# Kernel optimization log

Measured on AMD Instinct MI355X. Metric: run time of the kernel, lower is better.

## Reference

```python
import jax, jax.numpy as jnp
import numpy as np

E = 768      # embed_dim
H = 12       # num_heads
D = E // H   # head_dim = 64
G = 8        # num_groups (grouped 1x1 conv)
MAX_S = 197  # max_seq_len
RED = 8      # SE reduction ratio
S, B = 197, 64


def grouped_linear(x, w, b):
    """Grouped 1x1 conv as grouped linear. x: [..., Cin], w: [Cout, Cin//G], b: [Cout]."""
    cout = w.shape[0]
    cin = x.shape[-1]
    xg = x.reshape(x.shape[:-1] + (G, cin // G))
    wg = w.reshape(G, cout // G, cin // G)
    y = jnp.einsum('...gi,goi->...go', xg, wg)
    return y.reshape(x.shape[:-1] + (cout,)) + b


def channel_shuffle(x):
    """Shuffle channels (last dim) across G groups, matching torch channel_shuffle."""
    c = x.shape[-1]
    xg = x.reshape(x.shape[:-1] + (G, c // G))
    return jnp.swapaxes(xg, -1, -2).reshape(x.shape)


def layernorm(x, g, b, eps=1e-5):
    mu = jnp.mean(x, axis=-1, keepdims=True)
    var = jnp.var(x, axis=-1, keepdims=True)
    return (x - mu) * jax.lax.rsqrt(var + eps) * g + b


def setup_inputs() -> dict:
    rng = jax.random.key(0)
    ks = jax.random.split(rng, 16)
    std = 0.02
    return {
        'query': jax.random.normal(ks[0], (S, B, E), jnp.float32),
        'key':   jax.random.normal(ks[1], (S, B, E), jnp.float32),
        'value': jax.random.normal(ks[2], (S, B, E), jnp.float32),
        'qkv_w': jax.random.normal(ks[3], (3 * E, E // G), jnp.float32) * std,
        'qkv_b': jnp.zeros((3 * E,), jnp.float32),
        'out_w': jax.random.normal(ks[4], (E, E // G), jnp.float32) * std,
        'out_b': jnp.zeros((E,), jnp.float32),
        'rel_pos': jax.random.normal(ks[5], (2 * MAX_S - 1, D), jnp.float32) * std,
        'ln_g': jnp.ones((E,), jnp.float32),
        'ln_b': jnp.zeros((E,), jnp.float32),
        'fc1_w': jax.random.normal(ks[6], (E, E // RED), jnp.float32) * std,
        'fc1_b': jnp.zeros((E // RED,), jnp.float32),
        'fc2_w': jax.random.normal(ks[7], (E // RED, E), jnp.float32) * std,
        'fc2_b': jnp.zeros((E,), jnp.float32),
    }


def reference(query, key, value, qkv_w, qkv_b, out_w, out_b, rel_pos,
              ln_g, ln_b, fc1_w, fc1_b, fc2_w, fc2_b):
    seq_len, bsz, embed_dim = query.shape
    scaling = float(D) ** -0.5

    x = jnp.transpose(query, (1, 0, 2))              # [B, S, E]
    qkv = grouped_linear(x, qkv_w, qkv_b)            # [B, S, 3E]
    qkv = channel_shuffle(qkv)                       # [B, S, 3E]
    q, k, v = jnp.split(qkv, 3, axis=-1)             # each [B, S, E]

    def heads(t):                                    # [B, S, E] -> [B, H, S, D]
        return jnp.transpose(t.reshape(bsz, seq_len, H, D), (0, 2, 1, 3))
    q, k, v = heads(q) * scaling, heads(k), heads(v)

    attn_w = jnp.einsum('bhsd,bhtd->bhst', q, k)     # content-content

    # decoupled relative-position attention (note: slice, not skew, per source)
    rel = rel_pos[MAX_S - seq_len: MAX_S + seq_len - 1]           # [2S-1, D]
    content_pos = jnp.einsum('bhsd,rd->bhsr', q, rel)[..., seq_len - 1: 2 * seq_len - 1]
    pos_content = jnp.einsum('rd,bhtd->bhrt', rel, k)[:, :, seq_len - 1: 2 * seq_len - 1, :]
    attn_w = attn_w + content_pos + pos_content

    probs = jax.nn.softmax(attn_w, axis=-1)          # [B, H, S, S]
    attn = jnp.einsum('bhst,bhtd->bhsd', probs, v)   # [B, H, S, D]
    attn = jnp.transpose(attn, (0, 2, 1, 3)).reshape(bsz, seq_len, E)  # [B, S, E]

    # squeeze-excite style feature calibration gating
    scale = jax.nn.sigmoid(
        jnp.dot(jax.nn.gelu(jnp.dot(layernorm(attn, ln_g, ln_b), fc1_w) + fc1_b), fc2_w) + fc2_b)
    attn = attn * scale

    out = grouped_linear(attn, out_w, out_b)         # [B, S, E]
    out = jnp.transpose(out, (1, 0, 2))              # [S, B, E]

    avg_weights = jnp.sum(probs, axis=1) / H         # [B, S, S]
    return out, avg_weights
```

## Files before the change

kernel.cpp:

```cpp
#include <hip/hip_runtime.h>
#include <hip/hip_bf16.h>

constexpr int S = 197;
constexpr int B = 64;
constexpr int E = 768;
constexpr int H = 12;
constexpr int D = 64;
constexpr int M = S * B;
constexpr size_t SBE = (size_t)M * E;
constexpr int PST = 208;

typedef short bf16x8 __attribute__((ext_vector_type(8)));
typedef float f32x4 __attribute__((ext_vector_type(4)));
typedef unsigned int u32x4 __attribute__((ext_vector_type(4)));

__device__ __forceinline__ unsigned short f2b(float x) {
  unsigned int u = __float_as_uint(x);
  return (unsigned short)((u + 0x7FFFu + ((u >> 16) & 1u)) >> 16);
}
__device__ __forceinline__ float b2f(unsigned short u) {
  return __uint_as_float((unsigned int)u << 16);
}

__global__ __launch_bounds__(256) void mha_wprep(const float* __restrict__ w1,
                                                 const float* __restrict__ w2,
                                                 const float* __restrict__ lng,
                                                 const float* __restrict__ lnb,
                                                 const float* __restrict__ b1,
                                                 const float* __restrict__ rel,
                                                 const float* __restrict__ wq,
                                                 unsigned short* __restrict__ w1t,
                                                 unsigned short* __restrict__ w2t,
                                                 float* __restrict__ cgb,
                                                 float* __restrict__ cbb,
                                                 unsigned short* __restrict__ relb,
                                                 unsigned short* __restrict__ wqt) {
  const int bid = blockIdx.x, tid = threadIdx.x;
  if (bid < 288) {
    int idx = bid * 256 + tid;
    int n = idx / 768, k = idx - n * 768;
    w1t[idx] = f2b(lng[k] * w1[(size_t)k * 96 + n]);
  } else if (bid < 576) {
    int idx = (bid - 288) * 256 + tid;
    int n = idx / 96, k = idx - n * 96;
    w2t[idx] = f2b(w2[(size_t)k * 768 + n]);
  } else if (bid == 576) {
    if (tid < 96) {
      float cg = 0.f, cb = 0.f;
      for (int k = 0; k < 768; ++k) {
        float wv = w1[(size_t)k * 96 + tid];
        cg += lng[k] * wv;
        cb += lnb[k] * wv;
      }
      cgb[tid] = cg;
      cbb[tid] = cb + b1[tid];
    }
  } else if (bid < 641) {
    int idx = (bid - 577) * 256 + tid;
    int s2 = idx >> 6, d = idx & 63;
    float v = (s2 < S) ? rel[(size_t)(S - 1 + s2) * D + d] : 0.f;
    relb[idx] = f2b(v);
  } else {
    int idx = (bid - 641) * 256 + tid;
    wqt[idx] = f2b(wq[idx]);
  }
}

__global__ __launch_bounds__(256) void mha_xcvt(const float* __restrict__ x,
                                                unsigned short* __restrict__ xb) {
  size_t i = ((size_t)blockIdx.x * 256 + threadIdx.x) * 8;
  float4 v0 = *reinterpret_cast<const float4*>(x + i);
  float4 v1 = *reinterpret_cast<const float4*>(x + i + 4);
  unsigned short o[8] = {f2b(v0.x), f2b(v0.y), f2b(v0.z), f2b(v0.w),
                         f2b(v1.x), f2b(v1.y), f2b(v1.z), f2b(v1.w)};
  *(u32x4*)(xb + i) = *(const u32x4*)o;
}

__global__ __launch_bounds__(256) void mha_qkv_gemm(const unsigned short* __restrict__ xb,
                                                    const unsigned short* __restrict__ wqt,
                                                    const float* __restrict__ bias,
                                                    unsigned short* __restrict__ y) {
  const int m0 = blockIdx.x * 64;
  const int n0 = blockIdx.y * 96;
  const int g = blockIdx.y / 3;
  const int tid = threadIdx.x;
  const int lane = tid & 63, wv = tid >> 6;
  const int l15 = lane & 15, l4 = lane >> 4;

  const unsigned short* xr = xb + (size_t)(m0 + 16 * wv + l15) * E + g * 96 + l4 * 8;
  bf16x8 a0 = *(const bf16x8*)(xr);
  bf16x8 a1 = *(const bf16x8*)(xr + 32);
  bf16x8 a2 = *(const bf16x8*)(xr + 64);

  const int mloc = m0 + 16 * wv + 4 * l4;
#pragma unroll
  for (int nf = 0; nf < 6; ++nf) {
    const unsigned short* wr = wqt + (size_t)(n0 + nf * 16 + l15) * 96 + l4 * 8;
    f32x4 a = (f32x4){0.f, 0.f, 0.f, 0.f};
    a = __builtin_amdgcn_mfma_f32_16x16x32_bf16(a0, *(const bf16x8*)(wr), a, 0, 0, 0);
    a = __builtin_amdgcn_mfma_f32_16x16x32_bf16(a1, *(const bf16x8*)(wr + 32), a, 0, 0, 0);
    a = __builtin_amdgcn_mfma_f32_16x16x32_bf16(a2, *(const bf16x8*)(wr + 64), a, 0, 0, 0);
    int p = n0 + nf * 16 + l15;
    float bv = bias[p];
#pragma unroll
    for (int r = 0; r < 4; ++r)
      y[(size_t)(mloc + r) * 2304 + p] = f2b(a[r] + bv);
  }
}

__global__ __launch_bounds__(256) void mha_qkv_shuffle(const unsigned short* __restrict__ y,
                                                       const float* __restrict__ rel,
                                                       unsigned short* __restrict__ qb,
                                                       unsigned short* __restrict__ kb,
                                                       unsigned short* __restrict__ vb) {
  const int tid = threadIdx.x;
  const int lane = tid & 63;
  const int g = lane >> 3, j = lane & 7;
  const int d = j * 8 + g;
  const int wrow = tid >> 6;
  const int rbase = blockIdx.x * 16;

  float relv[4];
  int sA[4], bA[4];
#pragma unroll
  for (int r8 = 0; r8 < 4; ++r8) {
    int rowl = rbase + r8 * 4 + wrow;
    sA[r8] = rowl >> 6;
    bA[r8] = rowl & 63;
    relv[r8] = rel[(size_t)(S - 1 + sA[r8]) * D + d];
  }

  for (int h = 0; h < H; ++h) {
#pragma unroll
    for (int r8 = 0; r8 < 4; ++r8) {
      int rowl = rbase + r8 * 4 + wrow;
      const unsigned short* yr = y + (size_t)rowl * 2304 + g * 288 + h * 8 + j;
      size_t o = (((size_t)bA[r8] * H + h) * S + sA[r8]) * D + d;
      float vq = b2f(yr[0]);
      float vk = b2f(yr[96]);
      float vv = b2f(yr[192]);
      qb[o] = f2b(0.125f * vq + relv[r8]);
      kb[o] = f2b(vk + relv[r8]);
      vb[o] = f2b(vv);
    }
  }
}

__global__ __launch_bounds__(256) void mha_fattn(
    const unsigned short* __restrict__ qb, const unsigned short* __restrict__ kb,
    const unsigned short* __restrict__ vb, const unsigned short* __restrict__ relb,
    float* __restrict__ context, unsigned short* __restrict__ probs, int bh0) {
  __shared__ __align__(16) unsigned short KtPt[64 * 136];
  __shared__ __align__(16) unsigned short Vh[64 * 136];
  unsigned short* Kt = KtPt;
  unsigned short* Pt = KtPt;

  const int id = blockIdx.x;
  const int xcd = id & 7;
  const int rr = id >> 3;
  const int stile = rr & 3;
  const int bhl = xcd + 8 * (rr >> 2);
  const int bh = bh0 + bhl;
  const int b_ = bh / H, h_ = bh - b_ * H;
  const int s0 = stile * 64;
  const int tid = threadIdx.x;
  const int lane = tid & 63, w = tid >> 6;
  const int l15 = lane & 15, l4 = lane >> 4;
  const int vt = tid & 63;
  const int vdb = (tid >> 6) * 8;

  const unsigned short* qg = qb + (((size_t)bh * S + (s0 + 16 * w + l15)) << 6) + l4 * 8;
  const unsigned short* rg = relb + (((size_t)(s0 + 16 * w + l15)) << 6) + l4 * 8;
  bf16x8 aq0 = *(const bf16x8*)(qg);
  bf16x8 aq1 = *(const bf16x8*)(qg + 32);
  bf16x8 aq2 = *(const bf16x8*)(rg);
  bf16x8 aq3 = *(const bf16x8*)(rg + 32);

  auto loadK = [&](int tc, u32x4* kv, u32x4* rv) {
#pragma unroll
    for (int ii = 0; ii < 2; ++ii) {
      int idx = tid + ii * 256;
      int r = idx >> 3, c = idx & 7;
      int tg = tc * 64 + r;
      kv[ii] = (u32x4){0, 0, 0, 0};
      rv[ii] = (u32x4){0, 0, 0, 0};
      if (tg < S) {
        kv[ii] = *(const u32x4*)(kb + (((size_t)bh * S + tg) << 6) + c * 8);
        u32x4 rvv = *(const u32x4*)(relb + ((size_t)tg << 6) + c * 8);
        rv[ii] = rvv ^ 0x80008000u;
      }
    }
  };

  f32x4 acc[13];
#pragma unroll
  for (int i = 0; i < 13; ++i) acc[i] = (f32x4){0.f, 0.f, 0.f, 0.f};

  u32x4 kvA[2], rvA[2], kvB[2], rvB[2];
  loadK(0, kvA, rvA);

#pragma unroll
  for (int tc = 0; tc < 4; ++tc) {
    u32x4* kvc = (tc & 1) ? kvB : kvA;
    u32x4* rvc = (tc & 1) ? rvB : rvA;
#pragma unroll
    for (int ii = 0; ii < 2; ++ii) {
      int idx = tid + ii * 256;
      int r = idx >> 3, c = idx & 7;
      *(u32x4*)(Kt + r * 136 + c * 8) = kvc[ii];
      *(u32x4*)(Kt + r * 136 + 64 + c * 8) = rvc[ii];
    }
    if (tc < 3) loadK(tc + 1, (tc & 1) ? kvA : kvB, (tc & 1) ? rvA : rvB);
    __syncthreads();
#pragma unroll
    for (int tf = 0; tf < 4; ++tf) {
      if (tc == 3 && tf > 0) continue;
      const unsigned short* kbse = Kt + (tf * 16 + l15) * 136 + l4 * 8;
      f32x4 a = acc[tc * 4 + tf];
      a = __builtin_amdgcn_mfma_f32_16x16x32_bf16(aq0, *(const bf16x8*)(kbse), a, 0, 0, 0);
      a = __builtin_amdgcn_mfma_f32_16x16x32_bf16(aq1, *(const bf16x8*)(kbse + 32), a, 0, 0, 0);
      a = __builtin_amdgcn_mfma_f32_16x16x32_bf16(aq2, *(const bf16x8*)(kbse + 64), a, 0, 0, 0);
      a = __builtin_amdgcn_mfma_f32_16x16x32_bf16(aq3, *(const bf16x8*)(kbse + 96), a, 0, 0, 0);
      acc[tc * 4 + tf] = a;
    }
    __syncthreads();
  }

  u32x4 v1[4];
#pragma unroll
  for (int ii = 0; ii < 4; ++ii) {
    int t = (ii & 1) * 64 + vt;
    int d0 = vdb + (ii >> 1) * 32;
    v1[ii] = *(const u32x4*)(vb + (((size_t)bh * S + t) << 6) + d0);
  }

  if (l15 >= 5) acc[12] = (f32x4){-3.0e38f, -3.0e38f, -3.0e38f, -3.0e38f};
  float inv[4];
#pragma unroll
  for (int r = 0; r < 4; ++r) {
    float m = acc[0][r];
#pragma unroll
    for (int tf = 1; tf < 13; ++tf) m = fmaxf(m, acc[tf][r]);
#pragma unroll
    for (int off = 1; off < 16; off <<= 1) m = fmaxf(m, __shfl_xor(m, off, 64));
    float s = 0.f;
#pragma unroll
    for (int tf = 0; tf < 13; ++tf) {
      float e = __expf(acc[tf][r] - m);
      acc[tf][r] = e;
      s += e;
    }
#pragma unroll
    for (int off = 1; off < 16; off <<= 1) s += __shfl_xor(s, off, 64);
    inv[r] = 1.f / s;
  }

  f32x4 ov[4];
#pragma unroll
  for (int df = 0; df < 4; ++df) ov[df] = (f32x4){0.f, 0.f, 0.f, 0.f};

#pragma unroll
  for (int tf = 0; tf < 8; ++tf)
#pragma unroll
    for (int r = 0; r < 4; ++r)
      Pt[(16 * w + 4 * l4 + r) * 136 + tf * 16 + l15] = f2b(acc[tf][r] * inv[r]);
#pragma unroll
  for (int ii = 0; ii < 4; ++ii) {
    int t = (ii & 1) * 64 + vt;
    int d0 = vdb + (ii >> 1) * 32;
    const unsigned short* vp = (const unsigned short*)&v1[ii];
#pragma unroll
    for (int j = 0; j < 8; ++j) Vh[(d0 + j) * 136 + t] = vp[j];
  }
  __syncthreads();

  u32x4 v2[4];
#pragma unroll
  for (int ii = 0; ii < 4; ++ii) {
    int t = 128 + (ii & 1) * 64 + vt;
    int d0 = vdb + (ii >> 1) * 32;
    v2[ii] = (u32x4){0, 0, 0, 0};
    if (t < S) v2[ii] = *(const u32x4*)(vb + (((size_t)bh * S + t) << 6) + d0);
  }

  {
    const int r2 = tid >> 2;
    const int sg = s0 + r2;
    if (sg < S) {
#pragma unroll
      for (int j = 0; j < 4; ++j) {
        int c = (tid & 3) + 4 * j;
        u32x4 pv = *(const u32x4*)(Pt + r2 * 136 + c * 8);
        *(u32x4*)(probs + ((size_t)bhl * S + sg) * PST + c * 8) = pv;
      }
    }
  }
  {
    bf16x8 ap[4];
#pragma unroll
    for (int kf = 0; kf < 4; ++kf)
      ap[kf] = *(const bf16x8*)(Pt + (16 * w + l15) * 136 + kf * 32 + l4 * 8);
#pragma unroll
    for (int df = 0; df < 4; ++df) {
      const unsigned short* vbse = Vh + (df * 16 + l15) * 136 + l4 * 8;
      f32x4 o = ov[df];
#pragma unroll
      for (int kf = 0; kf < 4; ++kf)
        o = __builtin_amdgcn_mfma_f32_16x16x32_bf16(ap[kf], *(const bf16x8*)(vbse + kf * 32), o, 0, 0, 0);
      ov[df] = o;
    }
  }
  __syncthreads();

#pragma unroll
  for (int tf = 8; tf < 13; ++tf)
#pragma unroll
    for (int r = 0; r < 4; ++r)
      Pt[(16 * w + 4 * l4 + r) * 136 + (tf - 8) * 16 + l15] = f2b(acc[tf][r] * inv[r]);
#pragma unroll
  for (int r = 0; r < 4; ++r)
    Pt[(16 * w + 4 * l4 + r) * 136 + 80 + l15] = 0;
#pragma unroll
  for (int ii = 0; ii < 4; ++ii) {
    int t0h = (ii & 1) * 64 + vt;
    int d0 = vdb + (ii >> 1) * 32;
    if (t0h < 96) {
      const unsigned short* vp = (const unsigned short*)&v2[ii];
#pragma unroll
      for (int j = 0; j < 8; ++j) Vh[(d0 + j) * 136 + t0h] = vp[j];
    }
  }
  __syncthreads();

  {
    const int r2 = tid >> 2;
    const int sg = s0 + r2;
    if (sg < S) {
#pragma unroll
      for (int j = 0; j < 3; ++j) {
        int c = (tid & 3) + 4 * j;
        if (c < 10) {
          u32x4 pv = *(const u32x4*)(Pt + r2 * 136 + c * 8);
          *(u32x4*)(probs + ((size_t)bhl * S + sg) * PST + 128 + c * 8) = pv;
        }
      }
    }
  }
  {
    bf16x8 ap[3];
#pragma unroll
    for (int kf = 0; kf < 3; ++kf)
      ap[kf] = *(const bf16x8*)(Pt + (16 * w + l15) * 136 + kf * 32 + l4 * 8);
#pragma unroll
    for (int df = 0; df < 4; ++df) {
      const unsigned short* vbse = Vh + (df * 16 + l15) * 136 + l4 * 8;
      f32x4 o = ov[df];
#pragma unroll
      for (int kf = 0; kf < 3; ++kf)
        o = __builtin_amdgcn_mfma_f32_16x16x32_bf16(ap[kf], *(const bf16x8*)(vbse + kf * 32), o, 0, 0, 0);
      ov[df] = o;
    }
  }

#pragma unroll
  for (int df = 0; df < 4; ++df)
#pragma unroll
    for (int r = 0; r < 4; ++r) {
      int sg = s0 + 16 * w + 4 * l4 + r;
      if (sg < S)
        context[((size_t)b_ * S + sg) * E + h_ * 64 + df * 16 + l15] = ov[df][r];
    }
}

__global__ __launch_bounds__(256) void mha_avgred(const unsigned short* __restrict__ probs,
                                                  float* __restrict__ avg, int b0) {
  const int bs = blockIdx.x;
  const int bl = bs / S, s = bs - bl * S;
  const int t = threadIdx.x;
  if (t >= S) return;
  float acc = 0.f;
#pragma unroll
  for (int h = 0; h < H; ++h)
    acc += b2f(probs[(((size_t)bl * H + h) * S + s) * PST + t]);
  avg[(((size_t)(b0 + bl)) * S + s) * S + t] = acc * (1.f / H);
}

__global__ __launch_bounds__(128) void mha_fc1ln(const float* __restrict__ ctx,
                                                 const unsigned short* __restrict__ w1t,
                                                 const float* __restrict__ cgb,
                                                 const float* __restrict__ cbb,
                                                 unsigned short* __restrict__ h1) {
  __shared__ __align__(16) unsigned short As[32 * 104];
  __shared__ __align__(16) unsigned short Wl[48 * 104];
  __shared__ float smu[32], sinv[32];
  const int m0 = blockIdx.x * 32;
  const int n0 = blockIdx.y * 48;
  const int tid = threadIdx.x;
  const int lane = tid & 63, w = tid >> 6;
  const int l15 = lane & 15, l4 = lane >> 4;
  const int r = tid >> 2, q = tid & 3;

  float s1 = 0.f, s2 = 0.f;
  f32x4 acc[3];
#pragma unroll
  for (int nf = 0; nf < 3; ++nf) acc[nf] = (f32x4){0.f, 0.f, 0.f, 0.f};

  for (int c = 0; c < 8; ++c) {
    const int k0 = c * 96;
    {
      const float* xr = ctx + (size_t)(m0 + r) * E + k0 + q * 24;
      unsigned short* ar = As + r * 104 + q * 24;
#pragma unroll
      for (int j = 0; j < 6; ++j) {
        float4 v = *reinterpret_cast<const float4*>(xr + j * 4);
        s1 += v.x + v.y + v.z + v.w;
        s2 += v.x * v.x + v.y * v.y + v.z * v.z + v.w * v.w;
        ar[j * 4 + 0] = f2b(v.x); ar[j * 4 + 1] = f2b(v.y);
        ar[j * 4 + 2] = f2b(v.z); ar[j * 4 + 3] = f2b(v.w);
      }
    }
    for (int i = tid; i < 48 * 12; i += 128) {
      int n = i / 12, c8 = i - n * 12;
      *(u32x4*)(Wl + n * 104 + c8 * 8) =
          *(const u32x4*)(w1t + (size_t)(n0 + n) * E + k0 + c8 * 8);
    }
    __syncthreads();
    const unsigned short* arow = As + (16 * w + l15) * 104 + l4 * 8;
    bf16x8 a0 = *(const bf16x8*)(arow);
    bf16x8 a1 = *(const bf16x8*)(arow + 32);
    bf16x8 a2 = *(const bf16x8*)(arow + 64);
#pragma unroll
    for (int nf = 0; nf < 3; ++nf) {
      const unsigned short* wr = Wl + (nf * 16 + l15) * 104 + l4 * 8;
      f32x4 a = acc[nf];
      a = __builtin_amdgcn_mfma_f32_16x16x32_bf16(a0, *(const bf16x8*)(wr), a, 0, 0, 0);
      a = __builtin_amdgcn_mfma_f32_16x16x32_bf16(a1, *(const bf16x8*)(wr + 32), a, 0, 0, 0);
      a = __builtin_amdgcn_mfma_f32_16x16x32_bf16(a2, *(const bf16x8*)(wr + 64), a, 0, 0, 0);
      acc[nf] = a;
    }
    __syncthreads();
  }

  s1 += __shfl_xor(s1, 1, 64); s1 += __shfl_xor(s1, 2, 64);
  s2 += __shfl_xor(s2, 1, 64); s2 += __shfl_xor(s2, 2, 64);
  if (q == 0) {
    float mu = s1 * (1.f / E);
    float var = s2 * (1.f / E) - mu * mu;
    smu[r] = mu;
    sinv[r] = rsqrtf(var + 1e-5f);
  }
  __syncthreads();

#pragma unroll
  for (int nf = 0; nf < 3; ++nf) {
    int n = n0 + nf * 16 + l15;
    float cg = cgb[n], cb = cbb[n];
#pragma unroll
    for (int rr = 0; rr < 4; ++rr) {
      int ml = 16 * w + 4 * l4 + rr;
      float u = sinv[ml] * (acc[nf][rr] - smu[ml] * cg) + cb;
      float gl = 0.5f * u * (1.f + tanhf(0.7978845608028654f * (u + 0.044715f * u * u * u)));
      h1[(size_t)(m0 + ml) * 96 + n] = f2b(gl);
    }
  }
}

__global__ __launch_bounds__(256) void mha_fc2(const unsigned short* __restrict__ h1,
                                               const unsigned short* __restrict__ w2t,
                                               const float* __restrict__ bias,
                                               const float* __restrict__ ctx,
                                               unsigned short* __restrict__ attn2) {
  __shared__ __align__(16) unsigned short Hs[64 * 104];
  __shared__ __align__(16) unsigned short Wl[192 * 104];
  const int m0 = blockIdx.x * 64;
  const int n0 = blockIdx.y * 192;
  const int tid = threadIdx.x;
  const int lane = tid & 63, w = tid >> 6;
  const int l15 = lane & 15, l4 = lane >> 4;

  for (int i = tid; i < 64 * 12; i += 256) {
    int rr = i / 12, c8 = i - rr * 12;
    *(u32x4*)(Hs + rr * 104 + c8 * 8) =
        *(const u32x4*)(h1 + (size_t)(m0 + rr) * 96 + c8 * 8);
  }
  for (int i = tid; i < 192 * 12; i += 256) {
    int n = i / 12, c8 = i - n * 12;
    *(u32x4*)(Wl + n * 104 + c8 * 8) =
        *(const u32x4*)(w2t + (size_t)(n0 + n) * 96 + c8 * 8);
  }
  __syncthreads();

  const unsigned short* arow = Hs + (16 * w + l15) * 104 + l4 * 8;
  bf16x8 a0 = *(const bf16x8*)(arow);
  bf16x8 a1 = *(const bf16x8*)(arow + 32);
  bf16x8 a2 = *(const bf16x8*)(arow + 64);

#pragma unroll
  for (int nf = 0; nf < 12; ++nf) {
    const unsigned short* wr = Wl + (nf * 16 + l15) * 104 + l4 * 8;
    f32x4 a = (f32x4){0.f, 0.f, 0.f, 0.f};
    a = __builtin_amdgcn_mfma_f32_16x16x32_bf16(a0, *(const bf16x8*)(wr), a, 0, 0, 0);
    a = __builtin_amdgcn_mfma_f32_16x16x32_bf16(a1, *(const bf16x8*)(wr + 32), a, 0, 0, 0);
    a = __builtin_amdgcn_mfma_f32_16x16x32_bf16(a2, *(const bf16x8*)(wr + 64), a, 0, 0, 0);
    int n = n0 + nf * 16 + l15;
    float bv = bias[n];
#pragma unroll
    for (int rr = 0; rr < 4; ++rr) {
      int m = m0 + 16 * w + 4 * l4 + rr;
      float val = a[rr] + bv;
      float sg = 1.f / (1.f + __expf(-val));
      float cv = ctx[(size_t)m * E + n];
      attn2[(size_t)m * E + n] = f2b(cv * sg);
    }
  }
}

__global__ __launch_bounds__(256) void mha_out(const unsigned short* __restrict__ attn2,
                                               const float* __restrict__ w,
                                               const float* __restrict__ bias,
                                               float* __restrict__ outp) {
  __shared__ __align__(16) unsigned short Asl[64 * 104];
  __shared__ __align__(16) unsigned short Wl[96 * 104];
  __shared__ float bias_s[96];
  const int m0 = blockIdx.x * 64;
  const int g = blockIdx.y;
  const int n0 = g * 96;
  const int tid = threadIdx.x;
  const int lane = tid & 63, w_ = tid >> 6;
  const int l15 = lane & 15, l4 = lane >> 4;

  for (int i = tid; i < 64 * 12; i += 256) {
    int rr = i / 12, c8 = i - rr * 12;
    *(u32x4*)(Asl + rr * 104 + c8 * 8) =
        *(const u32x4*)(attn2 + (size_t)(m0 + rr) * E + n0 + c8 * 8);
  }
  for (int i = tid; i < 96 * 24; i += 256) {
    int n = i / 24, c4 = i - n * 24;
    float4 v = *reinterpret_cast<const float4*>(&w[(size_t)(n0 + n) * 96 + c4 * 4]);
    unsigned short* dst = Wl + n * 104 + c4 * 4;
    dst[0] = f2b(v.x); dst[1] = f2b(v.y); dst[2] = f2b(v.z); dst[3] = f2b(v.w);
  }
  if (tid < 96) bias_s[tid] = bias[n0 + tid];
  __syncthreads();

  const unsigned short* arow = Asl + (16 * w_ + l15) * 104 + l4 * 8;
  bf16x8 a0 = *(const bf16x8*)(arow);
  bf16x8 a1 = *(const bf16x8*)(arow + 32);
  bf16x8 a2 = *(const bf16x8*)(arow + 64);

  int bb4[4], ss4[4];
#pragma unroll
  for (int rr = 0; rr < 4; ++rr) {
    int m = m0 + 16 * w_ + 4 * l4 + rr;
    bb4[rr] = m / S;
    ss4[rr] = m - bb4[rr] * S;
  }

#pragma unroll
  for (int nf = 0; nf < 6; ++nf) {
    const unsigned short* wr = Wl + (nf * 16 + l15) * 104 + l4 * 8;
    f32x4 a = (f32x4){0.f, 0.f, 0.f, 0.f};
    a = __builtin_amdgcn_mfma_f32_16x16x32_bf16(a0, *(const bf16x8*)(wr), a, 0, 0, 0);
    a = __builtin_amdgcn_mfma_f32_16x16x32_bf16(a1, *(const bf16x8*)(wr + 32), a, 0, 0, 0);
    a = __builtin_amdgcn_mfma_f32_16x16x32_bf16(a2, *(const bf16x8*)(wr + 64), a, 0, 0, 0);
    int p = n0 + nf * 16 + l15;
    float bv = bias_s[p - n0];
#pragma unroll
    for (int rr = 0; rr < 4; ++rr)
      outp[((size_t)ss4[rr] * B + bb4[rr]) * E + p] = a[rr] + bv;
  }
}

extern "C" void kernel_launch(void* const* d_in, const int* in_sizes, int n_in,
                              void* d_out, int out_size, void* d_ws, size_t ws_size,
                              hipStream_t stream) {
  const float* query = (const float*)d_in[0];
  const float* qkv_w = (const float*)d_in[3];
  const float* qkv_b = (const float*)d_in[4];
  const float* out_w = (const float*)d_in[5];
  const float* out_b = (const float*)d_in[6];
  const float* rel   = (const float*)d_in[7];
  const float* ln_g  = (const float*)d_in[8];
  const float* ln_b  = (const float*)d_in[9];
  const float* fc1_w = (const float*)d_in[10];
  const float* fc1_b = (const float*)d_in[11];
  const float* fc2_w = (const float*)d_in[12];
  const float* fc2_b = (const float*)d_in[13];

  float* ws = (float*)d_ws;
  unsigned short* qb   = (unsigned short*)ws;
  unsigned short* xbuf = qb;
  unsigned short* kbuf = qb + SBE;
  unsigned short* vbb  = kbuf + SBE;
  unsigned short* relb = vbb + SBE;
  size_t off = 3 * SBE / 2 + 8192;
  float* context = ws + off;
  unsigned short* attn2b = (unsigned short*)(ws + off + SBE);
  unsigned short* ybuf = (unsigned short*)context;
  unsigned short* h1b = attn2b + SBE;
  unsigned short* w1t = h1b + (size_t)M * 96;
  unsigned short* w2t = w1t + 73728;
  unsigned short* wqt = w2t + 73728;
  float* cgb = (float*)(wqt + 221184);
  float* cbb = cgb + 96;
  unsigned short* probsb = (unsigned short*)(cbb + 96);
  float* outp = (float*)d_out;
  float* avgp = outp + SBE;

  size_t used_f = off + SBE + (SBE + (size_t)M * 96 + 368640) / 2 + 192;
  size_t avail_f = (ws_size / 4 > used_f) ? ws_size / 4 - used_f : 0;
  int Bc = 2;
  const int cand[6] = {64, 32, 16, 8, 4, 2};
  for (int i = 0; i < 6; ++i) {
    size_t need_f = ((size_t)cand[i] * H * S * PST + 1) / 2;
    if (need_f <= avail_f) { Bc = cand[i]; break; }
  }

  mha_wprep<<<1505, 256, 0, stream>>>(fc1_w, fc2_w, ln_g, ln_b, fc1_b, rel, qkv_w,
                                      w1t, w2t, cgb, cbb, relb, wqt);
  mha_xcvt<<<(int)(SBE / 8 / 256), 256, 0, stream>>>(query, xbuf);

  mha_qkv_gemm<<<dim3(M / 64, 24), 256, 0, stream>>>(xbuf, wqt, qkv_b, ybuf);
  mha_qkv_shuffle<<<M / 16, 256, 0, stream>>>(ybuf, rel, qb, kbuf, vbb);

  for (int b0 = 0; b0 < B; b0 += Bc) {
    int bc = (B - b0 < Bc) ? (B - b0) : Bc;
    int nbh = bc * H;
    mha_fattn<<<4 * nbh, 256, 0, stream>>>(qb, kbuf, vbb, relb, context, probsb,
                                           b0 * H);
    mha_avgred<<<bc * S, 256, 0, stream>>>(probsb, avgp, b0);
  }

  mha_fc1ln<<<dim3(M / 32, 2), 128, 0, stream>>>(context, w1t, cgb, cbb, h1b);
  mha_fc2<<<dim3(M / 64, 4), 256, 0, stream>>>(h1b, w2t, fc2_b, context, attn2b);
  mha_out<<<dim3(M / 64, 8), 256, 0, stream>>>(attn2b, out_w, out_b, outp);
}
```

Baseline: 257.3 us.

## Double attention block to 128 query rows with 512 threads sharing K/V tiles

The fused attention kernel now has each block cover 128 query rows with 8 waves instead of 64 rows with 4 waves. Staged K, rel and V tiles in shared memory are therefore reused by twice as many query rows, which halves redundant global loads and staging work per query. Each thread now loads one K/rel vector and two V vectors instead of two and four. The costs are twice the shared memory for the K/P buffer, fewer blocks in the grid, and a block size that may lower occupancy or raise barrier cost.

```diff
diff --git a/kernel.cpp b/kernel.cpp
--- a/kernel.cpp
+++ b/kernel.cpp
@@ -146,11 +146,11 @@
   }
 }
 
-__global__ __launch_bounds__(256) void mha_fattn(
+__global__ __launch_bounds__(512) void mha_fattn(
     const unsigned short* __restrict__ qb, const unsigned short* __restrict__ kb,
     const unsigned short* __restrict__ vb, const unsigned short* __restrict__ relb,
     float* __restrict__ context, unsigned short* __restrict__ probs, int bh0) {
-  __shared__ __align__(16) unsigned short KtPt[64 * 136];
+  __shared__ __align__(16) unsigned short KtPt[128 * 136];
   __shared__ __align__(16) unsigned short Vh[64 * 136];
   unsigned short* Kt = KtPt;
   unsigned short* Pt = KtPt;
@@ -158,11 +158,11 @@
   const int id = blockIdx.x;
   const int xcd = id & 7;
   const int rr = id >> 3;
-  const int stile = rr & 3;
-  const int bhl = xcd + 8 * (rr >> 2);
+  const int stile = rr & 1;
+  const int bhl = xcd + 8 * (rr >> 1);
   const int bh = bh0 + bhl;
   const int b_ = bh / H, h_ = bh - b_ * H;
-  const int s0 = stile * 64;
+  const int s0 = stile * 128;
   const int tid = threadIdx.x;
   const int lane = tid & 63, w = tid >> 6;
   const int l15 = lane & 15, l4 = lane >> 4;
@@ -170,25 +170,21 @@
   const int vdb = (tid >> 6) * 8;
 
   const unsigned short* qg = qb + (((size_t)bh * S + (s0 + 16 * w + l15)) << 6) + l4 * 8;
-  const unsigned short* rg = relb + (((size_t)(s0 + 16 * w + l15)) << 6) + l4 * 8;
+  const unsigned short* rg = relb + (((size_t)((s0 + 16 * w + l15) & 255)) << 6) + l4 * 8;
   bf16x8 aq0 = *(const bf16x8*)(qg);
   bf16x8 aq1 = *(const bf16x8*)(qg + 32);
   bf16x8 aq2 = *(const bf16x8*)(rg);
   bf16x8 aq3 = *(const bf16x8*)(rg + 32);
 
-  auto loadK = [&](int tc, u32x4* kv, u32x4* rv) {
-#pragma unroll
-    for (int ii = 0; ii < 2; ++ii) {
-      int idx = tid + ii * 256;
-      int r = idx >> 3, c = idx & 7;
-      int tg = tc * 64 + r;
-      kv[ii] = (u32x4){0, 0, 0, 0};
-      rv[ii] = (u32x4){0, 0, 0, 0};
-      if (tg < S) {
-        kv[ii] = *(const u32x4*)(kb + (((size_t)bh * S + tg) << 6) + c * 8);
-        u32x4 rvv = *(const u32x4*)(relb + ((size_t)tg << 6) + c * 8);
-        rv[ii] = rvv ^ 0x80008000u;
-      }
+  const int kr = tid >> 3, kc = tid & 7;
+  auto loadK = [&](int tc, u32x4& kv, u32x4& rv) {
+    int tg = tc * 64 + kr;
+    kv = (u32x4){0, 0, 0, 0};
+    rv = (u32x4){0, 0, 0, 0};
+    if (tg < S) {
+      kv = *(const u32x4*)(kb + (((size_t)bh * S + tg) << 6) + kc * 8);
+      u32x4 rvv = *(const u32x4*)(relb + ((size_t)tg << 6) + kc * 8);
+      rv = rvv ^ 0x80008000u;
     }
   };
 
@@ -196,21 +192,19 @@
 #pragma unroll
   for (int i = 0; i < 13; ++i) acc[i] = (f32x4){0.f, 0.f, 0.f, 0.f};
 
-  u32x4 kvA[2], rvA[2], kvB[2], rvB[2];
+  u32x4 kvA, rvA, kvB, rvB;
   loadK(0, kvA, rvA);
 
 #pragma unroll
   for (int tc = 0; tc < 4; ++tc) {
-    u32x4* kvc = (tc & 1) ? kvB : kvA;
-    u32x4* rvc = (tc & 1) ? rvB : rvA;
-#pragma unroll
-    for (int ii = 0; ii < 2; ++ii) {
-      int idx = tid + ii * 256;
-      int r = idx >> 3, c = idx & 7;
-      *(u32x4*)(Kt + r * 136 + c * 8) = kvc[ii];
-      *(u32x4*)(Kt + r * 136 + 64 + c * 8) = rvc[ii];
-    }
-    if (tc < 3) loadK(tc + 1, (tc & 1) ? kvA : kvB, (tc & 1) ? rvA : rvB);
+    u32x4 kvc = (tc & 1) ? kvB : kvA;
+    u32x4 rvc = (tc & 1) ? rvB : rvA;
+    *(u32x4*)(Kt + kr * 136 + kc * 8) = kvc;
+    *(u32x4*)(Kt + kr * 136 + 64 + kc * 8) = rvc;
+    if (tc < 3) {
+      if (tc & 1) loadK(tc + 1, kvA, rvA);
+      else        loadK(tc + 1, kvB, rvB);
+    }
     __syncthreads();
 #pragma unroll
     for (int tf = 0; tf < 4; ++tf) {
@@ -226,12 +220,11 @@
     __syncthreads();
   }
 
-  u32x4 v1[4];
-#pragma unroll
-  for (int ii = 0; ii < 4; ++ii) {
-    int t = (ii & 1) * 64 + vt;
-    int d0 = vdb + (ii >> 1) * 32;
-    v1[ii] = *(const u32x4*)(vb + (((size_t)bh * S + t) << 6) + d0);
+  u32x4 v1[2];
+#pragma unroll
+  for (int ii = 0; ii < 2; ++ii) {
+    int t = ii * 64 + vt;
+    v1[ii] = *(const u32x4*)(vb + (((size_t)bh * S + t) << 6) + vdb);
   }
 
   if (l15 >= 5) acc[12] = (f32x4){-3.0e38f, -3.0e38f, -3.0e38f, -3.0e38f};
@@ -265,22 +258,20 @@
     for (int r = 0; r < 4; ++r)
       Pt[(16 * w + 4 * l4 + r) * 136 + tf * 16 + l15] = f2b(acc[tf][r] * inv[r]);
 #pragma unroll
-  for (int ii = 0; ii < 4; ++ii) {
-    int t = (ii & 1) * 64 + vt;
-    int d0 = vdb + (ii >> 1) * 32;
+  for (int ii = 0; ii < 2; ++ii) {
+    int t = ii * 64 + vt;
     const unsigned short* vp = (const unsigned short*)&v1[ii];
 #pragma unroll
-    for (int j = 0; j < 8; ++j) Vh[(d0 + j) * 136 + t] = vp[j];
+    for (int j = 0; j < 8; ++j) Vh[(vdb + j) * 136 + t] = vp[j];
   }
   __syncthreads();
 
-  u32x4 v2[4];
-#pragma unroll
-  for (int ii = 0; ii < 4; ++ii) {
-    int t = 128 + (ii & 1) * 64 + vt;
-    int d0 = vdb + (ii >> 1) * 32;
+  u32x4 v2[2];
+#pragma unroll
+  for (int ii = 0; ii < 2; ++ii) {
+    int t = 128 + ii * 64 + vt;
     v2[ii] = (u32x4){0, 0, 0, 0};
-    if (t < S) v2[ii] = *(const u32x4*)(vb + (((size_t)bh * S + t) << 6) + d0);
+    if (t < S) v2[ii] = *(const u32x4*)(vb + (((size_t)bh * S + t) << 6) + vdb);
   }
 
   {
@@ -321,13 +312,12 @@
   for (int r = 0; r < 4; ++r)
     Pt[(16 * w + 4 * l4 + r) * 136 + 80 + l15] = 0;
 #pragma unroll
-  for (int ii = 0; ii < 4; ++ii) {
-    int t0h = (ii & 1) * 64 + vt;
-    int d0 = vdb + (ii >> 1) * 32;
+  for (int ii = 0; ii < 2; ++ii) {
+    int t0h = ii * 64 + vt;
     if (t0h < 96) {
       const unsigned short* vp = (const unsigned short*)&v2[ii];
 #pragma unroll
-      for (int j = 0; j < 8; ++j) Vh[(d0 + j) * 136 + t0h] = vp[j];
+      for (int j = 0; j < 8; ++j) Vh[(vdb + j) * 136 + t0h] = vp[j];
     }
   }
   __syncthreads();
@@ -626,7 +616,7 @@
   for (int b0 = 0; b0 < B; b0 += Bc) {
     int bc = (B - b0 < Bc) ? (B - b0) : Bc;
     int nbh = bc * H;
-    mha_fattn<<<4 * nbh, 256, 0, stream>>>(qb, kbuf, vbb, relb, context, probsb,
+    mha_fattn<<<2 * nbh, 512, 0, stream>>>(qb, kbuf, vbb, relb, context, probsb,
                                            b0 * H);
     mha_avgred<<<bc * S, 256, 0, stream>>>(probsb, avgp, b0);
   }
```

After: 259.2 us. No clear change (+0.7%).
